# Kernel optimization log

Hardware: AMD Instinct MI355X
Metric: run time of the kernel (lower is better)

## Reference

```python
import jax, jax.numpy as jnp
import numpy as np

B, D, K = 4, 128, 512   # batch, node_embedding_dim, num_nodes
ALPHA = 0.2             # LeakyReLU negative slope


def setup_inputs() -> dict:
    key = jax.random.key(0)
    k1, k2, k3, k4 = jax.random.split(key, 4)
    x = jax.random.normal(k1, (B, D, K), dtype=jnp.float32)
    # nn.Linear(2D -> D): store weight as (2D, D) for right-multiplication
    lin_w = jax.random.normal(k2, (2 * D, D), dtype=jnp.float32) * (1.0 / np.sqrt(2 * D))
    lin_b = jax.random.normal(k3, (D,), dtype=jnp.float32) * 0.01
    # attention vector a: (D,) (xavier-uniform in torch; scale-equivalent normal here)
    a = jax.random.normal(k4, (D,), dtype=jnp.float32) * (1.414 * np.sqrt(2.0 / (D + 1)))
    bias_mat = jnp.zeros((K, K), dtype=jnp.float32)  # init zeros per module
    return {"x": x, "lin_w": lin_w, "lin_b": lin_b, "a": a, "bias_mat": bias_mat}


def reference(x, lin_w, lin_b, a, bias_mat):
    # x: (B, D, K) -> transpose to (B, K, D); GATv2 path, residual = identity
    xt = jnp.swapaxes(x, 1, 2)                      # (B, K, D)
    d = xt.shape[-1]
    # lin(concat(v_i, v_j)) == v_i @ W1 + v_j @ W2 + b  (exact split; avoids (B,K,K,2D) concat)
    W1, W2 = lin_w[:d], lin_w[d:]
    left = xt @ W1 + lin_b                          # (B, K, D) -- v_i part (repeating block)
    right = xt @ W2                                 # (B, K, D) -- v_j part (alternating block)
    pre = left[:, :, None, :] + right[:, None, :, :]  # (B, K, K, D)
    h = jnp.where(pre > 0, pre, ALPHA * pre)        # LeakyReLU
    e = jnp.einsum('bijd,d->bij', h, a) + bias_mat  # (B, K, K)
    attn = jax.nn.softmax(e, axis=2)                # softmax over j (dropout p=0)
    agg = jnp.einsum('bij,bjd->bid', attn, xt)      # (B, K, D)
    out = jax.nn.sigmoid(agg) + xt                  # sigmoid + identity residual
    return jnp.swapaxes(out, 1, 2)                  # (B, D, K)
```

## Files before the change

### kernel.cpp

```cpp
#include <hip/hip_runtime.h>

#define B 4
#define D 128
#define K 512
#define TI 4

typedef __fp16 h2v __attribute__((ext_vector_type(2)));

__device__ __forceinline__ unsigned pkrtz(float a, float b) {
  h2v h = __builtin_amdgcn_cvt_pkrtz(a, b);
  union { h2v h; unsigned u; } c; c.h = h; return c.u;
}
__device__ __forceinline__ h2v u2h(unsigned u) {
  union { unsigned u; h2v h; } c; c.u = u; return c.h;
}
__device__ __forceinline__ float fdot2f(h2v a, h2v b, float c) {
#if __has_builtin(__builtin_amdgcn_fdot2)
  return __builtin_amdgcn_fdot2(a, b, c, false);
#else
  return c + (float)a.x * (float)b.x + (float)a.y * (float)b.y;
#endif
}
__device__ __forceinline__ h2v relu2(h2v a) {
#if __has_builtin(__builtin_elementwise_max)
  const h2v z = {(__fp16)0.f, (__fp16)0.f};
  return __builtin_elementwise_max(a, z);
#else
  h2v r;
  r.x = (float)a.x > 0.f ? a.x : (__fp16)0.f;
  r.y = (float)a.y > 0.f ? a.y : (__fp16)0.f;
  return r;
#endif
}

__global__ __launch_bounds__(256) void gat_lr16(
    const float* __restrict__ x, const float* __restrict__ lin_w,
    const float* __restrict__ lin_b, const float* __restrict__ a,
    unsigned* __restrict__ LhT, unsigned* __restrict__ RhT) {
  const int j0 = blockIdx.x * 64;
  const int E0 = blockIdx.y * 16;
  const int b = blockIdx.z;
  const int t = threadIdx.x;
  __shared__ float sx[D][64];
  __shared__ float sw1[D][16];
  __shared__ float sw2[D][16];
#pragma unroll
  for (int r = 0; r < 8; ++r) {
    const int fid = t + 256 * r;
    const int row = fid >> 4, c4 = fid & 15;
    *(float4*)&sx[row][4 * c4] =
        *(const float4*)&x[((size_t)b * D + row) * K + j0 + 4 * c4];
  }
#pragma unroll
  for (int r = 0; r < 8; ++r) {
    const int idx = t + 256 * r;
    const int row = idx >> 4, e = idx & 15;
    sw1[row][e] = lin_w[(size_t)row * D + E0 + e];
    sw2[row][e] = lin_w[(size_t)(D + row) * D + E0 + e];
  }
  __syncthreads();
  const int j = t & 63, g = t >> 6;
  float accL[4] = {0.f, 0.f, 0.f, 0.f}, accR[4] = {0.f, 0.f, 0.f, 0.f};
#pragma unroll 8
  for (int c = 0; c < D; ++c) {
    const float xv = sx[c][j];
    const float4 w1 = *(const float4*)&sw1[c][4 * g];
    const float4 w2 = *(const float4*)&sw2[c][4 * g];
    accL[0] = fmaf(xv, w1.x, accL[0]);
    accL[1] = fmaf(xv, w1.y, accL[1]);
    accL[2] = fmaf(xv, w1.z, accL[2]);
    accL[3] = fmaf(xv, w1.w, accL[3]);
    accR[0] = fmaf(xv, w2.x, accR[0]);
    accR[1] = fmaf(xv, w2.y, accR[1]);
    accR[2] = fmaf(xv, w2.z, accR[2]);
    accR[3] = fmaf(xv, w2.w, accR[3]);
  }
  const int e0 = E0 + 4 * g;
#pragma unroll
  for (int u = 0; u < 2; ++u) {
    const int ea = e0 + 2 * u, eb = ea + 1;
    const float uea = 0.8f * fabsf(a[ea]), ueb = 0.8f * fabsf(a[eb]);
    const float La = uea * (accL[2 * u] + lin_b[ea]);
    const float Lb = ueb * (accL[2 * u + 1] + lin_b[eb]);
    const float Ra = uea * accR[2 * u];
    const float Rb = ueb * accR[2 * u + 1];
    const size_t dp = (size_t)(ea >> 1);
    LhT[((size_t)b * (D / 2) + dp) * K + j0 + j] = pkrtz(La, Lb);
    RhT[((size_t)b * (D / 2) + dp) * K + j0 + j] = pkrtz(Ra, Rb);
  }
}

__global__ __launch_bounds__(256) void gat_attn16(
    const float* __restrict__ x, const float* __restrict__ a,
    const float* __restrict__ bias, const unsigned* __restrict__ LhT,
    const unsigned* __restrict__ RhT, float* __restrict__ out) {
  const int i0 = blockIdx.x * TI;
  const int b = blockIdx.y;
  const int t = threadIdx.x;
  __shared__ float sxt[D][TI];
  __shared__ unsigned slh[D / 2][TI];
  __shared__ unsigned ssg[D / 2];
  __shared__ float sSL[TI];
  __shared__ float seT[TI][K];

  {
    int idx = t;
    sxt[idx >> 2][idx & 3] = x[((size_t)b * D + (idx >> 2)) * K + i0 + (idx & 3)];
    idx = t + 256;
    sxt[idx >> 2][idx & 3] = x[((size_t)b * D + (idx >> 2)) * K + i0 + (idx & 3)];
    const int dp = t >> 2, ii = t & 3;
    slh[dp][ii] = LhT[((size_t)b * (D / 2) + dp) * K + i0 + ii];
    if (t < D / 2) {
      const float s0 = (a[2 * t] >= 0.f) ? 1.f : -1.f;
      const float s1 = (a[2 * t + 1] >= 0.f) ? 1.f : -1.f;
      ssg[t] = pkrtz(s0, s1);
    }
  }
  __syncthreads();
  {
    const int ii = t >> 6, dp = t & 63;
    float v = fdot2f(u2h(ssg[dp]), u2h(slh[dp][ii]), 0.f);
#pragma unroll
    for (int off = 32; off > 0; off >>= 1) v += __shfl_xor(v, off, 64);
    if ((t & 63) == 0) sSL[ii] = v;
  }
  __syncthreads();

  {
    const unsigned* rc = RhT + (size_t)b * (D / 2) * K;
    float accA[4] = {0.f, 0.f, 0.f, 0.f}, accB[4] = {0.f, 0.f, 0.f, 0.f};
    float srA = 0.f, srB = 0.f;
#pragma unroll 4
    for (int dp = 0; dp < D / 2; ++dp) {
      const unsigned ra = rc[(size_t)dp * K + t];
      const unsigned rb = rc[(size_t)dp * K + t + 256];
      const uint4 lh4 = *(const uint4*)&slh[dp][0];
      const h2v s2 = u2h(ssg[dp]);
      const h2v rva = u2h(ra), rvb = u2h(rb);
      srA = fdot2f(s2, rva, srA);
      srB = fdot2f(s2, rvb, srB);
      h2v l;
      l = u2h(lh4.x);
      accA[0] = fdot2f(s2, relu2(l + rva), accA[0]);
      accB[0] = fdot2f(s2, relu2(l + rvb), accB[0]);
      l = u2h(lh4.y);
      accA[1] = fdot2f(s2, relu2(l + rva), accA[1]);
      accB[1] = fdot2f(s2, relu2(l + rvb), accB[1]);
      l = u2h(lh4.z);
      accA[2] = fdot2f(s2, relu2(l + rva), accA[2]);
      accB[2] = fdot2f(s2, relu2(l + rvb), accB[2]);
      l = u2h(lh4.w);
      accA[3] = fdot2f(s2, relu2(l + rva), accA[3]);
      accB[3] = fdot2f(s2, relu2(l + rvb), accB[3]);
    }
#pragma unroll
    for (int ii = 0; ii < TI; ++ii) {
      seT[ii][t] = accA[ii] + 0.25f * (sSL[ii] + srA) +
                   bias[(size_t)(i0 + ii) * K + t];
      seT[ii][t + 256] = accB[ii] + 0.25f * (sSL[ii] + srB) +
                         bias[(size_t)(i0 + ii) * K + t + 256];
    }
  }
  __syncthreads();

  {
    const int w = t >> 6, lane = t & 63;
    float v[8];
    float m = -1e30f;
#pragma unroll
    for (int q = 0; q < 8; ++q) {
      v[q] = seT[w][lane + 64 * q];
      m = fmaxf(m, v[q]);
    }
#pragma unroll
    for (int off = 32; off > 0; off >>= 1) m = fmaxf(m, __shfl_xor(m, off, 64));
    float s = 0.f;
#pragma unroll
    for (int q = 0; q < 8; ++q) {
      v[q] = __expf(v[q] - m);
      s += v[q];
    }
#pragma unroll
    for (int off = 32; off > 0; off >>= 1) s += __shfl_xor(s, off, 64);
    const float inv = 1.f / s;
#pragma unroll
    for (int q = 0; q < 8; ++q) seT[w][lane + 64 * q] = v[q] * inv;
  }
  __syncthreads();

  {
    const int dg = t >> 1, jg = t & 1;
    float ag[4] = {0.f, 0.f, 0.f, 0.f};
    const float4* xr = (const float4*)(x + ((size_t)b * D + dg) * K);
#pragma unroll 4
    for (int q = 0; q < 64; ++q) {
      const int chunk = 2 * q + jg;
      const float4 xv = xr[chunk];
#pragma unroll
      for (int ii = 0; ii < TI; ++ii) {
        const float4 av = ((const float4*)&seT[ii][0])[chunk];
        ag[ii] = fmaf(av.x, xv.x, ag[ii]);
        ag[ii] = fmaf(av.y, xv.y, ag[ii]);
        ag[ii] = fmaf(av.z, xv.z, ag[ii]);
        ag[ii] = fmaf(av.w, xv.w, ag[ii]);
      }
    }
#pragma unroll
    for (int ii = 0; ii < TI; ++ii) ag[ii] += __shfl_xor(ag[ii], 1, 64);
    if (jg == 0) {
#pragma unroll
      for (int ii = 0; ii < TI; ++ii) {
        const float sg = 1.f / (1.f + __expf(-ag[ii]));
        out[((size_t)b * D + dg) * K + i0 + ii] = sg + sxt[dg][ii];
      }
    }
  }
}

#define ALPHA 0.2f
__global__ __launch_bounds__(512) void gat_fused(
    const float* __restrict__ x, const float* __restrict__ lin_w,
    const float* __restrict__ lin_b, const float* __restrict__ a,
    const float* __restrict__ bias, float* __restrict__ out) {
  const int i = blockIdx.x, b = blockIdx.y, t = threadIdx.x;
  __shared__ float sxi[D], sLi[D], sa[D];
  __shared__ float lpart[4 * D];
  __shared__ float xtT[D * 64];
  __shared__ float epars[8 * 64];
  __shared__ float se[K];
  __shared__ float sattn[K], spart[K];
  __shared__ float sred[8];

  if (t < D) {
    sxi[t] = x[((size_t)b * D + t) * K + i];
    sa[t] = a[t];
  }
  __syncthreads();
  {
    const int c = t & (D - 1), q = t >> 7;
    float acc = 0.f;
    const float* W1 = lin_w + c;
#pragma unroll 8
    for (int d = q * 32; d < q * 32 + 32; ++d)
      acc = fmaf(sxi[d], W1[(size_t)d * D], acc);
    lpart[q * D + c] = acc;
  }
  __syncthreads();
  if (t < D)
    sLi[t] = lin_b[t] + lpart[t] + lpart[D + t] + lpart[2 * D + t] +
             lpart[3 * D + t];
  __syncthreads();

  for (int jt = 0; jt < K / 64; ++jt) {
    const int j0 = jt * 64;
    for (int idx = t; idx < D * 64; idx += 512)
      xtT[idx] = x[((size_t)b * D + (idx >> 6)) * K + j0 + (idx & 63)];
    __syncthreads();
    const int jj = t & 63, g = t >> 6, dp0 = g * 16;
    float accv[16];
#pragma unroll
    for (int v = 0; v < 16; ++v) accv[v] = 0.f;
    for (int dc = 0; dc < D; dc += 16) {
      float xv[16];
#pragma unroll
      for (int u = 0; u < 16; ++u) xv[u] = xtT[(dc + u) * 64 + jj];
#pragma unroll
      for (int u = 0; u < 16; ++u) {
        const float* W2r = lin_w + (size_t)(D + dc + u) * D + dp0;
#pragma unroll
        for (int v = 0; v < 16; ++v) accv[v] = fmaf(xv[u], W2r[v], accv[v]);
      }
    }
    float ep = 0.f;
#pragma unroll
    for (int v = 0; v < 16; ++v) {
      const float pre = sLi[dp0 + v] + accv[v];
      ep = fmaf(sa[dp0 + v], pre > 0.f ? pre : ALPHA * pre, ep);
    }
    epars[g * 64 + jj] = ep;
    __syncthreads();
    if (t < 64) {
      float esum = bias[(size_t)i * K + j0 + t];
#pragma unroll
      for (int g2 = 0; g2 < 8; ++g2) esum += epars[g2 * 64 + t];
      se[j0 + t] = esum;
    }
    __syncthreads();
  }

  float e = se[t];
  float m = e;
#pragma unroll
  for (int off = 32; off > 0; off >>= 1) m = fmaxf(m, __shfl_xor(m, off, 64));
  if ((t & 63) == 0) sred[t >> 6] = m;
  __syncthreads();
  m = sred[0];
#pragma unroll
  for (int w = 1; w < 8; ++w) m = fmaxf(m, sred[w]);
  const float ev = __expf(e - m);
  float s = ev;
#pragma unroll
  for (int off = 32; off > 0; off >>= 1) s += __shfl_xor(s, off, 64);
  __syncthreads();
  if ((t & 63) == 0) sred[t >> 6] = s;
  __syncthreads();
  s = 0.f;
#pragma unroll
  for (int w = 0; w < 8; ++w) s += sred[w];
  sattn[t] = ev * (1.f / s);
  __syncthreads();

  const int d = t >> 2, c = t & 3;
  const float4* X4 = (const float4*)(x + ((size_t)b * D + d) * K);
  const float4* A4 = (const float4*)sattn;
  float p = 0.f;
#pragma unroll 4
  for (int q = 0; q < K / 16; ++q) {
    const int idx = c + 4 * q;
    float4 xv = X4[idx], av = A4[idx];
    p = fmaf(av.x, xv.x, p);
    p = fmaf(av.y, xv.y, p);
    p = fmaf(av.z, xv.z, p);
    p = fmaf(av.w, xv.w, p);
  }
  spart[t] = p;
  __syncthreads();
  if (t < D) {
    const float agg =
        spart[4 * t] + spart[4 * t + 1] + spart[4 * t + 2] + spart[4 * t + 3];
    const float sg = 1.f / (1.f + __expf(-agg));
    out[((size_t)b * D + t) * K + i] = sg + sxi[t];
  }
}

extern "C" void kernel_launch(void* const* d_in, const int* in_sizes, int n_in,
                              void* d_out, int out_size, void* d_ws,
                              size_t ws_size, hipStream_t stream) {
  const float* x = (const float*)d_in[0];
  const float* lin_w = (const float*)d_in[1];
  const float* lin_b = (const float*)d_in[2];
  const float* a = (const float*)d_in[3];
  const float* bias = (const float*)d_in[4];
  float* out = (float*)d_out;

  const size_t half_words = (size_t)B * (D / 2) * K;
  const size_t need = 2 * half_words * sizeof(unsigned);
  if (ws_size >= need && d_ws != nullptr) {
    unsigned* LhT = (unsigned*)d_ws;
    unsigned* RhT = LhT + half_words;
    gat_lr16<<<dim3(K / 64, D / 16, B), 256, 0, stream>>>(x, lin_w, lin_b, a,
                                                          LhT, RhT);
    gat_attn16<<<dim3(K / TI, B), 256, 0, stream>>>(x, a, bias, LhT, RhT, out);
  } else {
    gat_fused<<<dim3(K, B), 512, 0, stream>>>(x, lin_w, lin_b, a, bias, out);
  }
}
```

Baseline: 87.03 us.

## Use fp16 x copy and packed fp16 attention for aggregation with fdot2

The first kernel now also writes an fp16 packed copy of x. The attention kernel stores softmax weights as packed fp16 and computes the aggregation with fdot2 over 128-bit loads, and it swaps the old per-thread float4 loop for a wave-level reduction. It also changes the j-to-thread mapping so R values and bias are read as paired loads. The aim is to halve the bytes of x read per block in the aggregation phase and double the math rate, at the cost of extra workspace, an extra write in the first kernel and reduced precision in the aggregation.

```diff
diff --git a/kernel.cpp b/kernel.cpp
--- a/kernel.cpp
+++ b/kernel.cpp
@@ -36,7 +36,8 @@
 __global__ __launch_bounds__(256) void gat_lr16(
     const float* __restrict__ x, const float* __restrict__ lin_w,
     const float* __restrict__ lin_b, const float* __restrict__ a,
-    unsigned* __restrict__ LhT, unsigned* __restrict__ RhT) {
+    unsigned* __restrict__ LhT, unsigned* __restrict__ RhT,
+    unsigned* __restrict__ XhT) {
   const int j0 = blockIdx.x * 64;
   const int E0 = blockIdx.y * 16;
   const int b = blockIdx.z;
@@ -59,6 +60,15 @@
     sw2[row][e] = lin_w[(size_t)(D + row) * D + E0 + e];
   }
   __syncthreads();
+  if (E0 == 0) {
+#pragma unroll
+    for (int r = 0; r < 16; ++r) {
+      const int idx = t + 256 * r;
+      const int row = idx >> 5, jc = idx & 31;
+      XhT[((size_t)b * D + row) * (K / 2) + (j0 >> 1) + jc] =
+          pkrtz(sx[row][2 * jc], sx[row][2 * jc + 1]);
+    }
+  }
   const int j = t & 63, g = t >> 6;
   float accL[4] = {0.f, 0.f, 0.f, 0.f}, accR[4] = {0.f, 0.f, 0.f, 0.f};
 #pragma unroll 8
@@ -93,7 +103,8 @@
 __global__ __launch_bounds__(256) void gat_attn16(
     const float* __restrict__ x, const float* __restrict__ a,
     const float* __restrict__ bias, const unsigned* __restrict__ LhT,
-    const unsigned* __restrict__ RhT, float* __restrict__ out) {
+    const unsigned* __restrict__ RhT, const unsigned* __restrict__ XhT,
+    float* __restrict__ out) {
   const int i0 = blockIdx.x * TI;
   const int b = blockIdx.y;
   const int t = threadIdx.x;
@@ -102,6 +113,7 @@
   __shared__ unsigned ssg[D / 2];
   __shared__ float sSL[TI];
   __shared__ float seT[TI][K];
+  __shared__ unsigned sattn16[TI][K / 2];
 
   {
     int idx = t;
@@ -132,11 +144,10 @@
     float srA = 0.f, srB = 0.f;
 #pragma unroll 4
     for (int dp = 0; dp < D / 2; ++dp) {
-      const unsigned ra = rc[(size_t)dp * K + t];
-      const unsigned rb = rc[(size_t)dp * K + t + 256];
+      const uint2 rr = *(const uint2*)&rc[(size_t)dp * K + 2 * t];
       const uint4 lh4 = *(const uint4*)&slh[dp][0];
       const h2v s2 = u2h(ssg[dp]);
-      const h2v rva = u2h(ra), rvb = u2h(rb);
+      const h2v rva = u2h(rr.x), rvb = u2h(rr.y);
       srA = fdot2f(s2, rva, srA);
       srB = fdot2f(s2, rvb, srB);
       h2v l;
@@ -155,63 +166,64 @@
     }
 #pragma unroll
     for (int ii = 0; ii < TI; ++ii) {
-      seT[ii][t] = accA[ii] + 0.25f * (sSL[ii] + srA) +
-                   bias[(size_t)(i0 + ii) * K + t];
-      seT[ii][t + 256] = accB[ii] + 0.25f * (sSL[ii] + srB) +
-                         bias[(size_t)(i0 + ii) * K + t + 256];
+      const float2 bv = *(const float2*)&bias[(size_t)(i0 + ii) * K + 2 * t];
+      float2 ev;
+      ev.x = accA[ii] + 0.25f * (sSL[ii] + srA) + bv.x;
+      ev.y = accB[ii] + 0.25f * (sSL[ii] + srB) + bv.y;
+      *(float2*)&seT[ii][2 * t] = ev;
     }
   }
   __syncthreads();
 
   {
     const int w = t >> 6, lane = t & 63;
-    float v[8];
+    float2 v[4];
     float m = -1e30f;
 #pragma unroll
-    for (int q = 0; q < 8; ++q) {
-      v[q] = seT[w][lane + 64 * q];
-      m = fmaxf(m, v[q]);
+    for (int q = 0; q < 4; ++q) {
+      v[q] = *(const float2*)&seT[w][2 * lane + 128 * q];
+      m = fmaxf(m, fmaxf(v[q].x, v[q].y));
     }
 #pragma unroll
     for (int off = 32; off > 0; off >>= 1) m = fmaxf(m, __shfl_xor(m, off, 64));
     float s = 0.f;
 #pragma unroll
-    for (int q = 0; q < 8; ++q) {
-      v[q] = __expf(v[q] - m);
-      s += v[q];
+    for (int q = 0; q < 4; ++q) {
+      v[q].x = __expf(v[q].x - m);
+      v[q].y = __expf(v[q].y - m);
+      s += v[q].x + v[q].y;
     }
 #pragma unroll
     for (int off = 32; off > 0; off >>= 1) s += __shfl_xor(s, off, 64);
     const float inv = 1.f / s;
 #pragma unroll
-    for (int q = 0; q < 8; ++q) seT[w][lane + 64 * q] = v[q] * inv;
-  }
-  __syncthreads();
-
-  {
-    const int dg = t >> 1, jg = t & 1;
-    float ag[4] = {0.f, 0.f, 0.f, 0.f};
-    const float4* xr = (const float4*)(x + ((size_t)b * D + dg) * K);
-#pragma unroll 4
-    for (int q = 0; q < 64; ++q) {
-      const int chunk = 2 * q + jg;
-      const float4 xv = xr[chunk];
-#pragma unroll
-      for (int ii = 0; ii < TI; ++ii) {
-        const float4 av = ((const float4*)&seT[ii][0])[chunk];
-        ag[ii] = fmaf(av.x, xv.x, ag[ii]);
-        ag[ii] = fmaf(av.y, xv.y, ag[ii]);
-        ag[ii] = fmaf(av.z, xv.z, ag[ii]);
-        ag[ii] = fmaf(av.w, xv.w, ag[ii]);
+    for (int q = 0; q < 4; ++q)
+      sattn16[w][lane + 64 * q] = pkrtz(v[q].x * inv, v[q].y * inv);
+  }
+  __syncthreads();
+
+  {
+    const int l = t & 63, w = t >> 6;
+    const int iL = l & 3, cg = l >> 2;
+    const unsigned* xh = XhT + (size_t)b * D * (K / 2);
+    for (int r = 0; r < 32; ++r) {
+      const int d = w * 32 + r;
+      float acc = 0.f;
+#pragma unroll
+      for (int q = 0; q < 4; ++q) {
+        const int c8 = cg + 16 * q;
+        const uint4 xp = *(const uint4*)&xh[(size_t)d * (K / 2) + 4 * c8];
+        const uint4 ap = *(const uint4*)&sattn16[iL][4 * c8];
+        acc = fdot2f(u2h(ap.x), u2h(xp.x), acc);
+        acc = fdot2f(u2h(ap.y), u2h(xp.y), acc);
+        acc = fdot2f(u2h(ap.z), u2h(xp.z), acc);
+        acc = fdot2f(u2h(ap.w), u2h(xp.w), acc);
       }
-    }
-#pragma unroll
-    for (int ii = 0; ii < TI; ++ii) ag[ii] += __shfl_xor(ag[ii], 1, 64);
-    if (jg == 0) {
-#pragma unroll
-      for (int ii = 0; ii < TI; ++ii) {
-        const float sg = 1.f / (1.f + __expf(-ag[ii]));
-        out[((size_t)b * D + dg) * K + i0 + ii] = sg + sxt[dg][ii];
+#pragma unroll
+      for (int off = 4; off < 64; off <<= 1) acc += __shfl_xor(acc, off, 64);
+      if (cg == 0) {
+        const float sg = 1.f / (1.f + __expf(-acc));
+        out[((size_t)b * D + d) * K + i0 + iL] = sg + sxt[d][iL];
       }
     }
   }
@@ -344,13 +356,16 @@
   float* out = (float*)d_out;
 
   const size_t half_words = (size_t)B * (D / 2) * K;
-  const size_t need = 2 * half_words * sizeof(unsigned);
+  const size_t xh_words = (size_t)B * D * (K / 2);
+  const size_t need = (2 * half_words + xh_words) * sizeof(unsigned);
   if (ws_size >= need && d_ws != nullptr) {
     unsigned* LhT = (unsigned*)d_ws;
     unsigned* RhT = LhT + half_words;
+    unsigned* XhT = RhT + half_words;
     gat_lr16<<<dim3(K / 64, D / 16, B), 256, 0, stream>>>(x, lin_w, lin_b, a,
-                                                          LhT, RhT);
-    gat_attn16<<<dim3(K / TI, B), 256, 0, stream>>>(x, a, bias, LhT, RhT, out);
+                                                          LhT, RhT, XhT);
+    gat_attn16<<<dim3(K / TI, B), 256, 0, stream>>>(x, a, bias, LhT, RhT, XhT,
+                                                    out);
   } else {
     gat_fused<<<dim3(K, B), 512, 0, stream>>>(x, lin_w, lin_b, a, bias, out);
   }
```

New measurement: 96.47 us. 1.11x slower.
